# Kernel tuning notes

Measured on AMD Instinct MI355X. Metric: run time of the kernel, lower is better.

Reference implementation:

```python
import jax, jax.numpy as jnp
import numpy as np

B, N, F, H, D = 4096, 14, 768, 1, 768  # batch, num_diseases, feature_dim, num_heads, hidden_dim
L = 3  # number of GAT layers


def setup_inputs() -> dict:
    key = jax.random.key(0)
    ks = jax.random.split(key, 8)
    features = jax.random.normal(ks[0], (B, N, F), dtype=jnp.float32)
    # random adjacency mask; ensure nonzero diagonal so no row is fully masked
    mask = (jax.random.uniform(ks[1], (B, N, N)) > 0.3).astype(jnp.float32)
    adj = jnp.maximum(mask, jnp.eye(N, dtype=jnp.float32))
    W_emb = jax.random.normal(ks[2], (F, D), dtype=jnp.float32) / np.sqrt(F)
    b_emb = jnp.zeros((D,), dtype=jnp.float32)
    gat_W = jax.random.normal(ks[3], (L, D, H * D), dtype=jnp.float32) / np.sqrt(D)
    gat_a = jax.random.normal(ks[4], (L, 2 * D, H), dtype=jnp.float32) / np.sqrt(2 * D)
    W_out = jax.random.normal(ks[5], (H * D, F), dtype=jnp.float32) / np.sqrt(H * D)
    b_out = jnp.zeros((F,), dtype=jnp.float32)
    return dict(features=features, adj=adj, W_emb=W_emb, b_emb=b_emb,
                gat_W=gat_W, gat_a=gat_a, W_out=W_out, b_out=b_out)


def _gat_layer(x, adj, W, a):
    # x: [B, N, D], W: [D, H*D], a: [2D, H]
    Bm, Nn = x.shape[0], x.shape[1]
    Wh = (x @ W).reshape(Bm, Nn, H, D)
    # e[b,i,j,h] = Wh[b,i,h] . a[:D,h] + Wh[b,j,h] . a[D:,h]  (concat attention, un-materialized)
    a_i, a_j = a[:D], a[D:]
    ei = jnp.einsum('bnhd,dh->bnh', Wh, a_i)
    ej = jnp.einsum('bnhd,dh->bnh', Wh, a_j)
    e = ei[:, :, None, :] + ej[:, None, :, :]  # [B, N, N, H]
    e = jnp.where(adj[..., None] > 0, e, jnp.float32(-1e30))  # masked_fill(-inf)
    attn = jax.nn.softmax(e, axis=2)  # softmax over j (dim=2), matches torch
    h = jnp.einsum('bijh,bjhd->bihd', attn, Wh)  # attention-weighted aggregation
    return h.reshape(Bm, Nn, H * D), attn  # concat=True output


def reference(features, adj, W_emb, b_emb, gat_W, gat_a, W_out, b_out):
    # dropout layers are identity at inference
    x = features @ W_emb + b_emb  # disease_embedding
    attns = []
    for l in range(L):
        x, attn = _gat_layer(x, adj, gat_W[l], gat_a[l])
        attns.append(attn)
        if l < L - 1:
            x = jax.nn.elu(x)
    out = x @ W_out + b_out  # output_proj
    return (out, attns[0], attns[1], attns[2])
```

## Files before the change

kernel.cpp:

```cpp
#include <hip/hip_runtime.h>

typedef unsigned short u16;
typedef float f32x4 __attribute__((ext_vector_type(4)));
typedef short bf16x8 __attribute__((ext_vector_type(8)));
typedef unsigned short u16x8 __attribute__((ext_vector_type(8)));

#define ND 768
#define KD 768

__device__ __forceinline__ float bf2f(u16 u) {
    union { unsigned i; float f; } v; v.i = ((unsigned)u) << 16; return v.f;
}
__device__ __forceinline__ u16 f2bf(float f) {
    union { float f; unsigned u; } x; x.f = f;
    unsigned r = x.u + 0x7fffu + ((x.u >> 16) & 1u);
    return (u16)(r >> 16);
}
__device__ __forceinline__ void async16(const void* g, void* l) {
    __builtin_amdgcn_global_load_lds((const __attribute__((address_space(1))) void*)g,
                                     (__attribute__((address_space(3))) void*)l, 16, 0, 0);
}

__global__ __launch_bounds__(256) void conv_w(const float* __restrict__ W_emb,
                                              const float* __restrict__ gat_W,
                                              const float* __restrict__ W_out,
                                              u16* __restrict__ Wt)
{
    __shared__ float lds[64][65];
    const int m  = blockIdx.x / 144;
    const int r  = blockIdx.x % 144;
    const int tr = r / 12;
    const int tc = r % 12;
    const float* src = (m == 0) ? W_emb : (m <= 3) ? (gat_W + (size_t)(m - 1) * 589824) : W_out;
    const int c  = threadIdx.x & 63;
    const int w4 = threadIdx.x >> 6;
    #pragma unroll
    for (int i = 0; i < 16; ++i) {
        int kk = i * 4 + w4;
        lds[kk][c] = src[(size_t)(tr * 64 + kk) * 768 + tc * 64 + c];
    }
    __syncthreads();
    u16* dst = Wt + (size_t)m * 589824;
    #pragma unroll
    for (int i = 0; i < 16; ++i) {
        int nn = i * 4 + w4;
        dst[(size_t)(tc * 64 + nn) * 768 + tr * 64 + c] = f2bf(lds[c][nn]);
    }
}

__global__ __launch_bounds__(256) void conv_x(const float4* __restrict__ in,
                                              u16* __restrict__ outp, int n4)
{
    for (int i = blockIdx.x * 256 + threadIdx.x; i < n4; i += gridDim.x * 256) {
        float4 v = in[i];
        union { u16 s[4]; uint2 u; } o;
        o.s[0] = f2bf(v.x); o.s[1] = f2bf(v.y); o.s[2] = f2bf(v.z); o.s[3] = f2bf(v.w);
        ((uint2*)outp)[i] = o.u;
    }
}

template<bool F32OUT>
__global__ __launch_bounds__(256) void gemm_bt(const u16* __restrict__ A,
                                               const u16* __restrict__ Bt,
                                               const float* __restrict__ bias,
                                               void* __restrict__ Cout)
{
    __shared__ u16 lds2[2][2][4096];
    const int tid  = threadIdx.x;
    const int lane = tid & 63;
    const int wvb  = tid & ~63;
    const int wm   = ((tid >> 7) & 1) * 64;
    const int wn   = ((tid >> 6) & 1) * 64;
    const int wg = blockIdx.x;
    const int id = (wg & 7) * 336 + (wg >> 3);
    const int tn = (id % 6) * 128;
    const int tm = (id / 6) * 128;

    f32x4 acc[4][4] = {};

    const int lr = lane & 15;
    const int lk = (((lane >> 4) ^ ((lr >> 1) & 3)) << 3);

    const int row0 = tid >> 2;
    const int kc0  = (((tid & 3) ^ ((tid >> 3) & 3)) << 3);
    const u16* aSrc = A  + (size_t)(tm + row0) * KD + kc0;
    const u16* bSrc = Bt + (size_t)(tn + row0) * KD + kc0;

    #define STAGE(b, ks_) { const int k0 = (ks_) * 32;                      \
        async16(aSrc + k0,                  &lds2[b][0][wvb * 8]);          \
        async16(aSrc + (size_t)64 * KD + k0, &lds2[b][0][(256 + wvb) * 8]); \
        async16(bSrc + k0,                  &lds2[b][1][wvb * 8]);          \
        async16(bSrc + (size_t)64 * KD + k0, &lds2[b][1][(256 + wvb) * 8]); }

    STAGE(0, 0);

    #pragma unroll 2
    for (int ks = 0; ks < KD / 32; ++ks) {
        const int cur = ks & 1;
        if (ks + 1 < KD / 32) {
            STAGE(cur ^ 1, ks + 1);
            asm volatile("s_waitcnt vmcnt(4)" ::: "memory");
        } else {
            asm volatile("s_waitcnt vmcnt(0)" ::: "memory");
        }
        __builtin_amdgcn_s_barrier();
        asm volatile("" ::: "memory");

        const u16* As = lds2[cur][0];
        const u16* Bs = lds2[cur][1];
        bf16x8 af[4], bf[4];
        #pragma unroll
        for (int mi = 0; mi < 4; ++mi)
            af[mi] = *(const bf16x8*)&As[(wm + mi * 16 + lr) * 32 + lk];
        #pragma unroll
        for (int ni = 0; ni < 4; ++ni)
            bf[ni] = *(const bf16x8*)&Bs[(wn + ni * 16 + lr) * 32 + lk];
        #pragma unroll
        for (int mi = 0; mi < 4; ++mi)
            #pragma unroll
            for (int ni = 0; ni < 4; ++ni)
                acc[mi][ni] = __builtin_amdgcn_mfma_f32_16x16x32_bf16(
                    af[mi], bf[ni], acc[mi][ni], 0, 0, 0);

        if (ks + 1 < KD / 32) {
            asm volatile("" ::: "memory");
            __builtin_amdgcn_s_barrier();
        }
    }
    #undef STAGE

    const int lr4 = (lane >> 4) << 2;
    #pragma unroll
    for (int ni = 0; ni < 4; ++ni) {
        int col = tn + wn + ni * 16 + lr;
        float bv = bias ? bias[col] : 0.0f;
        #pragma unroll
        for (int mi = 0; mi < 4; ++mi) {
            int rowb = tm + wm + mi * 16 + lr4;
            #pragma unroll
            for (int r = 0; r < 4; ++r) {
                float v = acc[mi][ni][r] + bv;
                if (F32OUT)
                    ((float*)Cout)[(size_t)(rowb + r) * ND + col] = v;
                else
                    ((u16*)Cout)[(size_t)(rowb + r) * ND + col] = f2bf(v);
            }
        }
    }
}

template<bool ELU>
__global__ __launch_bounds__(256) void gat_mix(const u16* __restrict__ Wh,
                                               const float* __restrict__ adj,
                                               const float* __restrict__ avec,
                                               float* __restrict__ attn_out,
                                               u16* __restrict__ Xout)
{
    __shared__ u16 wh[14 * 768];
    __shared__ float s_ei[14], s_ej[14];
    __shared__ float s_attn[196];
    const int b = blockIdx.x;
    const int tid = threadIdx.x;
    const u16* whb = Wh + (size_t)b * 10752;

    for (int c = tid; c < 1344; c += 256)
        ((uint4*)wh)[c] = ((const uint4*)whb)[c];
    __syncthreads();

    if (tid < 224) {
        const int i = tid >> 4, l = tid & 15;
        float ai = 0.f, aj = 0.f;
        #pragma unroll
        for (int c = 0; c < 6; ++c) {
            int d = c * 128 + l * 8;
            u16x8 v  = *(const u16x8*)&wh[i * 768 + d];
            float4 x0 = *(const float4*)&avec[d];
            float4 x1 = *(const float4*)&avec[d + 4];
            float4 y0 = *(const float4*)&avec[768 + d];
            float4 y1 = *(const float4*)&avec[768 + d + 4];
            float w0 = bf2f(v[0]), w1 = bf2f(v[1]), w2 = bf2f(v[2]), w3 = bf2f(v[3]);
            float w4 = bf2f(v[4]), w5 = bf2f(v[5]), w6 = bf2f(v[6]), w7 = bf2f(v[7]);
            ai += w0*x0.x + w1*x0.y + w2*x0.z + w3*x0.w + w4*x1.x + w5*x1.y + w6*x1.z + w7*x1.w;
            aj += w0*y0.x + w1*y0.y + w2*y0.z + w3*y0.w + w4*y1.x + w5*y1.y + w6*y1.z + w7*y1.w;
        }
        #pragma unroll
        for (int off = 8; off; off >>= 1) {
            ai += __shfl_xor(ai, off);
            aj += __shfl_xor(aj, off);
        }
        if (l == 0) { s_ei[i] = ai; s_ej[i] = aj; }
    }
    __syncthreads();

    if (tid < 14) {
        const int i = tid;
        float e[14];
        float mx = -3.0e38f;
        #pragma unroll
        for (int j = 0; j < 14; ++j) {
            float ev = (adj[(size_t)b * 196 + i * 14 + j] > 0.f) ? (s_ei[i] + s_ej[j]) : -1.0e30f;
            e[j] = ev; mx = fmaxf(mx, ev);
        }
        float sum = 0.f;
        #pragma unroll
        for (int j = 0; j < 14; ++j) { float pp = __expf(e[j] - mx); e[j] = pp; sum += pp; }
        float inv = 1.0f / sum;
        #pragma unroll
        for (int j = 0; j < 14; ++j) s_attn[i * 14 + j] = e[j] * inv;
    }
    __syncthreads();

    if (tid < 196) attn_out[(size_t)b * 196 + tid] = s_attn[tid];

    for (int pp = tid; pp < 14 * 48; pp += 256) {
        const int i  = pp / 48;
        const int d0 = (pp % 48) * 16;
        float acc[16] = {};
        #pragma unroll
        for (int j = 0; j < 14; ++j) {
            float aw = s_attn[i * 14 + j];
            u16x8 wv0 = *(const u16x8*)&wh[j * 768 + d0];
            u16x8 wv1 = *(const u16x8*)&wh[j * 768 + d0 + 8];
            #pragma unroll
            for (int qq = 0; qq < 8; ++qq) {
                acc[qq]     += aw * bf2f(wv0[qq]);
                acc[8 + qq] += aw * bf2f(wv1[qq]);
            }
        }
        union { u16 s[16]; uint4 u[2]; } o;
        #pragma unroll
        for (int qq = 0; qq < 16; ++qq) {
            float v = acc[qq];
            if (ELU && v < 0.f) v = __expf(v) - 1.0f;
            o.s[qq] = f2bf(v);
        }
        *(uint4*)&Xout[(size_t)b * 10752 + i * 768 + d0]     = o.u[0];
        *(uint4*)&Xout[(size_t)b * 10752 + i * 768 + d0 + 8] = o.u[1];
    }
}

extern "C" void kernel_launch(void* const* d_in, const int* in_sizes, int n_in,
                              void* d_out, int out_size, void* d_ws, size_t ws_size,
                              hipStream_t stream)
{
    const float* features = (const float*)d_in[0];
    const float* adj      = (const float*)d_in[1];
    const float* W_emb    = (const float*)d_in[2];
    const float* b_emb    = (const float*)d_in[3];
    const float* gat_W    = (const float*)d_in[4];
    const float* gat_a    = (const float*)d_in[5];
    const float* W_out    = (const float*)d_in[6];
    const float* b_out    = (const float*)d_in[7];
    float* out = (float*)d_out;

    u16* Wh = (u16*)d_ws;
    u16* Wt = Wh + 44040192;
    u16* H0 = (u16*)d_out;
    u16* H1 = H0 + 44040192;
    float* attn0 = out + 44040192;
    float* attn1 = attn0 + 802816;
    float* attn2 = attn1 + 802816;

    conv_w<<<dim3(720), 256, 0, stream>>>(W_emb, gat_W, W_out, Wt);
    conv_x<<<dim3(4096), 256, 0, stream>>>((const float4*)features, H0, 11010048);

    dim3 gg(2688);
    gemm_bt<false><<<gg, 256, 0, stream>>>(H0, Wt, b_emb, H1);
    gemm_bt<false><<<gg, 256, 0, stream>>>(H1, Wt + 589824, nullptr, Wh);
    gat_mix<true><<<dim3(4096), 256, 0, stream>>>(Wh, adj, gat_a, attn0, H0);
    gemm_bt<false><<<gg, 256, 0, stream>>>(H0, Wt + 2 * 589824, nullptr, Wh);
    gat_mix<true><<<dim3(4096), 256, 0, stream>>>(Wh, adj, gat_a + 1536, attn1, H1);
    gemm_bt<false><<<gg, 256, 0, stream>>>(H1, Wt + 3 * 589824, nullptr, Wh);
    gat_mix<false><<<dim3(4096), 256, 0, stream>>>(Wh, adj, gat_a + 3072, attn2, Wh);
    gemm_bt<true><<<gg, 256, 0, stream>>>(Wh, Wt + 4 * 589824, b_out, (void*)out);
}
```

Before: 702.3 us.

## Replace 128x128 GEMM with 256x256-tile 8-wave kernel using 4-stage async pipeline

The bf16 GEMM moves from 128x128 tiles with 4 waves and double buffering to 256x256 tiles with 8 waves per block and a 4-deep LDS ring of async global-to-LDS loads. Each k-step's MFMAs are split into two halves that are interleaved with staging the A and B tiles, and s_setprio raises wave priority around the MFMA bursts. The goal is more data reuse per byte loaded and better overlap of memory with compute. The cost is 128 KB of LDS per block, a 128-float accumulator per thread, and only 672 blocks, which may not balance evenly across CUs.

```diff
diff --git a/kernel.cpp b/kernel.cpp
--- a/kernel.cpp
+++ b/kernel.cpp
@@ -60,86 +60,106 @@
 }
 
 template<bool F32OUT>
-__global__ __launch_bounds__(256) void gemm_bt(const u16* __restrict__ A,
-                                               const u16* __restrict__ Bt,
-                                               const float* __restrict__ bias,
-                                               void* __restrict__ Cout)
-{
-    __shared__ u16 lds2[2][2][4096];
+__global__ __launch_bounds__(512, 2) void gemm8p(const u16* __restrict__ A,
+                                                 const u16* __restrict__ Bt,
+                                                 const float* __restrict__ bias,
+                                                 void* __restrict__ Cout)
+{
+    __shared__ u16 lds[4 * 16384];
     const int tid  = threadIdx.x;
     const int lane = tid & 63;
-    const int wvb  = tid & ~63;
-    const int wm   = ((tid >> 7) & 1) * 64;
-    const int wn   = ((tid >> 6) & 1) * 64;
+    const int wid  = tid >> 6;
+    const int wr   = wid >> 2;
+    const int wc   = wid & 3;
     const int wg = blockIdx.x;
-    const int id = (wg & 7) * 336 + (wg >> 3);
-    const int tn = (id % 6) * 128;
-    const int tm = (id / 6) * 128;
-
-    f32x4 acc[4][4] = {};
-
-    const int lr = lane & 15;
-    const int lk = (((lane >> 4) ^ ((lr >> 1) & 3)) << 3);
-
+    const int id = (wg & 7) * 84 + (wg >> 3);
+    const int tm = (id / 3) * 256;
+    const int tn = (id % 3) * 256;
+
+    const int lr  = lane & 15;
+    const int lsl = lane >> 4;
+    const int lk  = ((lsl ^ ((lr >> 1) & 3)) << 3);
+    const int offA0 = (wr * 128 + lr) * 32 + lk;
+    const int offB0 = (wc * 64 + lr) * 32 + lk;
+
+    const int wvb8 = (tid & ~63) * 8;
+    const int kc0  = (((tid & 3) ^ ((tid >> 3) & 3)) << 3);
     const int row0 = tid >> 2;
-    const int kc0  = (((tid & 3) ^ ((tid >> 3) & 3)) << 3);
-    const u16* aSrc = A  + (size_t)(tm + row0) * KD + kc0;
-    const u16* bSrc = Bt + (size_t)(tn + row0) * KD + kc0;
-
-    #define STAGE(b, ks_) { const int k0 = (ks_) * 32;                      \
-        async16(aSrc + k0,                  &lds2[b][0][wvb * 8]);          \
-        async16(aSrc + (size_t)64 * KD + k0, &lds2[b][0][(256 + wvb) * 8]); \
-        async16(bSrc + k0,                  &lds2[b][1][wvb * 8]);          \
-        async16(bSrc + (size_t)64 * KD + k0, &lds2[b][1][(256 + wvb) * 8]); }
-
-    STAGE(0, 0);
-
-    #pragma unroll 2
-    for (int ks = 0; ks < KD / 32; ++ks) {
-        const int cur = ks & 1;
-        if (ks + 1 < KD / 32) {
-            STAGE(cur ^ 1, ks + 1);
-            asm volatile("s_waitcnt vmcnt(4)" ::: "memory");
-        } else {
-            asm volatile("s_waitcnt vmcnt(0)" ::: "memory");
-        }
-        __builtin_amdgcn_s_barrier();
-        asm volatile("" ::: "memory");
-
-        const u16* As = lds2[cur][0];
-        const u16* Bs = lds2[cur][1];
-        bf16x8 af[4], bf[4];
-        #pragma unroll
-        for (int mi = 0; mi < 4; ++mi)
-            af[mi] = *(const bf16x8*)&As[(wm + mi * 16 + lr) * 32 + lk];
-        #pragma unroll
-        for (int ni = 0; ni < 4; ++ni)
-            bf[ni] = *(const bf16x8*)&Bs[(wn + ni * 16 + lr) * 32 + lk];
-        #pragma unroll
-        for (int mi = 0; mi < 4; ++mi)
-            #pragma unroll
-            for (int ni = 0; ni < 4; ++ni)
-                acc[mi][ni] = __builtin_amdgcn_mfma_f32_16x16x32_bf16(
-                    af[mi], bf[ni], acc[mi][ni], 0, 0, 0);
-
-        if (ks + 1 < KD / 32) {
-            asm volatile("" ::: "memory");
-            __builtin_amdgcn_s_barrier();
-        }
-    }
-    #undef STAGE
-
-    const int lr4 = (lane >> 4) << 2;
+    const u16* aS0 = A  + (size_t)(tm + row0) * KD + kc0;
+    const u16* aS1 = aS0 + (size_t)128 * KD;
+    const u16* bS0 = Bt + (size_t)(tn + row0) * KD + kc0;
+    const u16* bS1 = bS0 + (size_t)128 * KD;
+
+    f32x4 acc[8][4] = {};
+
+#define STAGE_A(s_, t_) { u16* d = &lds[(s_) * 16384 + wvb8]; const int k0 = (t_) * 32; \
+        async16(aS0 + k0, d); async16(aS1 + k0, d + 4096); }
+#define STAGE_B(s_, t_) { u16* d = &lds[(s_) * 16384 + 8192 + wvb8]; const int k0 = (t_) * 32; \
+        async16(bS0 + k0, d); async16(bS1 + k0, d + 4096); }
+
+    STAGE_A(0, 0) STAGE_B(0, 0)
+    STAGE_A(1, 1) STAGE_B(1, 1)
+    STAGE_A(2, 2) STAGE_B(2, 2)
+    asm volatile("s_waitcnt vmcnt(8)" ::: "memory");
+    __builtin_amdgcn_s_barrier();
+    asm volatile("" ::: "memory");
+
+    #pragma unroll 1
+    for (int t = 0; t < 24; ++t) {
+        const u16* As = &lds[(t & 3) * 16384];
+        const u16* Bs = As + 8192;
+        bf16x8 af[8], bf[4];
+        #pragma unroll
+        for (int mf = 0; mf < 8; ++mf)
+            af[mf] = *(const bf16x8*)&As[offA0 + mf * 512];
+        bf[0] = *(const bf16x8*)&Bs[offB0];
+        bf[1] = *(const bf16x8*)&Bs[offB0 + 512];
+        if (t + 3 < 24) STAGE_A((t + 3) & 3, t + 3)
+        __builtin_amdgcn_s_barrier();
+        asm volatile("" ::: "memory");
+        __builtin_amdgcn_s_setprio(1);
+        #pragma unroll
+        for (int mf = 0; mf < 8; ++mf) {
+            acc[mf][0] = __builtin_amdgcn_mfma_f32_16x16x32_bf16(af[mf], bf[0], acc[mf][0], 0, 0, 0);
+            acc[mf][1] = __builtin_amdgcn_mfma_f32_16x16x32_bf16(af[mf], bf[1], acc[mf][1], 0, 0, 0);
+        }
+        __builtin_amdgcn_s_setprio(0);
+        __builtin_amdgcn_s_barrier();
+        asm volatile("" ::: "memory");
+        bf[2] = *(const bf16x8*)&Bs[offB0 + 1024];
+        bf[3] = *(const bf16x8*)&Bs[offB0 + 1536];
+        if (t + 3 < 24) STAGE_B((t + 3) & 3, t + 3)
+        if (t < 23) {
+            if (t <= 20)      asm volatile("s_waitcnt vmcnt(8)" ::: "memory");
+            else if (t == 21) asm volatile("s_waitcnt vmcnt(4)" ::: "memory");
+            else              asm volatile("s_waitcnt vmcnt(0)" ::: "memory");
+        }
+        __builtin_amdgcn_s_barrier();
+        asm volatile("" ::: "memory");
+        __builtin_amdgcn_s_setprio(1);
+        #pragma unroll
+        for (int mf = 0; mf < 8; ++mf) {
+            acc[mf][2] = __builtin_amdgcn_mfma_f32_16x16x32_bf16(af[mf], bf[2], acc[mf][2], 0, 0, 0);
+            acc[mf][3] = __builtin_amdgcn_mfma_f32_16x16x32_bf16(af[mf], bf[3], acc[mf][3], 0, 0, 0);
+        }
+        __builtin_amdgcn_s_setprio(0);
+        __builtin_amdgcn_s_barrier();
+        asm volatile("" ::: "memory");
+    }
+#undef STAGE_A
+#undef STAGE_B
+
+    const int lr4 = lsl << 2;
     #pragma unroll
-    for (int ni = 0; ni < 4; ++ni) {
-        int col = tn + wn + ni * 16 + lr;
+    for (int nf = 0; nf < 4; ++nf) {
+        int col = tn + wc * 64 + nf * 16 + lr;
         float bv = bias ? bias[col] : 0.0f;
         #pragma unroll
-        for (int mi = 0; mi < 4; ++mi) {
-            int rowb = tm + wm + mi * 16 + lr4;
+        for (int mf = 0; mf < 8; ++mf) {
+            int rowb = tm + wr * 128 + mf * 16 + lr4;
             #pragma unroll
             for (int r = 0; r < 4; ++r) {
-                float v = acc[mi][ni][r] + bv;
+                float v = acc[mf][nf][r] + bv;
                 if (F32OUT)
                     ((float*)Cout)[(size_t)(rowb + r) * ND + col] = v;
                 else
@@ -264,13 +284,13 @@
     conv_w<<<dim3(720), 256, 0, stream>>>(W_emb, gat_W, W_out, Wt);
     conv_x<<<dim3(4096), 256, 0, stream>>>((const float4*)features, H0, 11010048);
 
-    dim3 gg(2688);
-    gemm_bt<false><<<gg, 256, 0, stream>>>(H0, Wt, b_emb, H1);
-    gemm_bt<false><<<gg, 256, 0, stream>>>(H1, Wt + 589824, nullptr, Wh);
+    dim3 gg(672);
+    gemm8p<false><<<gg, 512, 0, stream>>>(H0, Wt, b_emb, H1);
+    gemm8p<false><<<gg, 512, 0, stream>>>(H1, Wt + 589824, nullptr, Wh);
     gat_mix<true><<<dim3(4096), 256, 0, stream>>>(Wh, adj, gat_a, attn0, H0);
-    gemm_bt<false><<<gg, 256, 0, stream>>>(H0, Wt + 2 * 589824, nullptr, Wh);
+    gemm8p<false><<<gg, 512, 0, stream>>>(H0, Wt + 2 * 589824, nullptr, Wh);
     gat_mix<true><<<dim3(4096), 256, 0, stream>>>(Wh, adj, gat_a + 1536, attn1, H1);
-    gemm_bt<false><<<gg, 256, 0, stream>>>(H1, Wt + 3 * 589824, nullptr, Wh);
+    gemm8p<false><<<gg, 512, 0, stream>>>(H1, Wt + 3 * 589824, nullptr, Wh);
     gat_mix<false><<<dim3(4096), 256, 0, stream>>>(Wh, adj, gat_a + 3072, attn2, Wh);
-    gemm_bt<true><<<gg, 256, 0, stream>>>(Wh, Wt + 4 * 589824, b_out, (void*)out);
-}
+    gemm8p<true><<<gg, 512, 0, stream>>>(Wh, Wt + 4 * 589824, b_out, (void*)out);
+}
```

Measured after the change: 744.8 us. +6.0%, slower.
